# Kernel optimization log

Hardware: AMD Instinct MI355X
Metric: run time of the kernel (lower is better)

## Reference

```python
import jax, jax.numpy as jnp
import numpy as np

NHEAD = 16

def setup_inputs() -> dict:
    key = jax.random.key(0)
    k0, k1, k2, k3 = jax.random.split(key, 4)
    d = 2048
    hd = d // NHEAD
    x = jax.random.normal(k0, (4, 2048, d), dtype=jnp.float32)
    Wq = jax.random.normal(k1, (d, d), dtype=jnp.float32) * (d ** -0.5)
    Wkv = jax.random.normal(k2, (d, 2 * hd), dtype=jnp.float32) * (d ** -0.5)
    Wo = jax.random.normal(k3, (d, d), dtype=jnp.float32) * (d ** -0.5)
    return {"x": x, "Wq": Wq, "Wkv": Wkv, "Wo": Wo}


def reference(x, Wq, Wkv, Wo):
    # Multi-query attention: h query heads share a single K/V head.
    b, n, d = x.shape
    h = NHEAD
    hd = d // h
    scale = hd ** -0.5
    q = (x @ Wq).reshape(b, n, h, hd) * scale      # (b, n, h, hd)
    kv = x @ Wkv                                    # (b, n, 2*hd) -- self-attention (context == input)
    k, v = kv[..., :hd], kv[..., hd:]               # shared single KV head: (b, t, hd)
    sim = jnp.einsum('bnhd,btd->bhnt', q, k)        # (b, h, n, t)
    att = jax.nn.softmax(sim, axis=-1)              # dropout_p = 0.0 (eval)
    y = jnp.einsum('bhnt,btd->bhnd', att, v)        # (b, h, n, hd)
    y = jnp.transpose(y, (0, 2, 1, 3)).reshape(b, n, d)  # 'b h n d -> b n (h d)'
    return y @ Wo
```

## Files before the change

kernel.cpp:

```cpp
#include <hip/hip_runtime.h>

typedef short short8 __attribute__((ext_vector_type(8)));
typedef float f32x4 __attribute__((ext_vector_type(4)));
typedef float f32x16 __attribute__((ext_vector_type(16)));
typedef unsigned int u32x4 __attribute__((ext_vector_type(4)));

#define B_   4
#define N_   2048
#define D_   2048
#define H_   16
#define HD_  128
#define M_   (B_ * N_)
#define KVC  256
#define NQKV (D_ + KVC)

__device__ __forceinline__ unsigned short f2bf(float f) {
  unsigned u = __builtin_bit_cast(unsigned, f);
  u = (u + 0x7FFFu + ((u >> 16) & 1u)) >> 16;
  return (unsigned short)u;
}

__device__ __forceinline__ void gl2lds16(const void* g, void* l) {
  __builtin_amdgcn_global_load_lds((const __attribute__((address_space(1))) void*)g,
                                   (__attribute__((address_space(3))) void*)l,
                                   16, 0, 0);
}

__device__ __forceinline__ unsigned cvt_pk_bf16(float lo, float hi) {
  unsigned r;
  asm volatile("v_cvt_pk_bf16_f32 %0, %1, %2" : "=v"(r) : "v"(lo), "v"(hi));
  return r;
}

#define LGKM0 do { asm volatile("s_waitcnt lgkmcnt(0)" ::: "memory"); \
                   __builtin_amdgcn_sched_barrier(0); } while (0)
#define BAR   do { __builtin_amdgcn_sched_barrier(0); __builtin_amdgcn_s_barrier(); \
                   __builtin_amdgcn_sched_barrier(0); } while (0)

__global__ __launch_bounds__(256) void cvt_bf16_kernel(const float* __restrict__ in,
                                                       unsigned short* __restrict__ out,
                                                       int n8) {
  int i = blockIdx.x * 256 + threadIdx.x;
  if (i >= n8) return;
  float4 a = ((const float4*)in)[i * 2];
  float4 b = ((const float4*)in)[i * 2 + 1];
  u32x4 u;
  u[0] = cvt_pk_bf16(a.x, a.y);
  u[1] = cvt_pk_bf16(a.z, a.w);
  u[2] = cvt_pk_bf16(b.x, b.y);
  u[3] = cvt_pk_bf16(b.z, b.w);
  ((short8*)out)[i] = __builtin_bit_cast(short8, u);
}

__global__ __launch_bounds__(256) void transpose_cvt(const float* __restrict__ in,
                                                     unsigned short* __restrict__ out,
                                                     int R, int C) {
  __shared__ float tile[64][65];
  int r0 = blockIdx.x * 64, c0 = blockIdx.y * 64;
  int t = threadIdx.x;
  int tr = t >> 4, tc4 = (t & 15) * 4;
#pragma unroll
  for (int it = 0; it < 4; ++it) {
    int r = it * 16 + tr;
    float4 v = *(const float4*)(in + (size_t)(r0 + r) * C + c0 + tc4);
    tile[r][tc4 + 0] = v.x; tile[r][tc4 + 1] = v.y;
    tile[r][tc4 + 2] = v.z; tile[r][tc4 + 3] = v.w;
  }
  __syncthreads();
#pragma unroll
  for (int it = 0; it < 4; ++it) {
    int oc = it * 16 + tr;
    ushort4 o;
    o.x = f2bf(tile[tc4 + 0][oc]);
    o.y = f2bf(tile[tc4 + 1][oc]);
    o.z = f2bf(tile[tc4 + 2][oc]);
    o.w = f2bf(tile[tc4 + 3][oc]);
    *(ushort4*)(out + (size_t)(c0 + oc) * R + r0 + tc4) = o;
  }
}

__global__ __launch_bounds__(256) void transpose_v(const unsigned short* __restrict__ kv,
                                                   unsigned short* __restrict__ vt) {
  __shared__ unsigned short tile[64][72];
  int t0 = blockIdx.x * 64, d0 = blockIdx.y * 64, b = blockIdx.z;
  int tid = threadIdx.x;
  int tr = tid >> 3, tc8 = (tid & 7) * 8;
#pragma unroll
  for (int it = 0; it < 2; ++it) {
    int r = it * 32 + tr;
    short8 v = *(const short8*)(kv + (size_t)(b * N_ + t0 + r) * KVC + HD_ + d0 + tc8);
#pragma unroll
    for (int j = 0; j < 8; ++j) tile[r][tc8 + j] = (unsigned short)v[j];
  }
  __syncthreads();
  int beta0 = tc8 >> 2, beta1 = beta0 + 1;
  int p0 = (((beta0 & 3) == 1) || ((beta0 & 3) == 2)) ? (beta0 ^ 3) : beta0;
  int p1 = (((beta1 & 3) == 1) || ((beta1 & 3) == 2)) ? (beta1 ^ 3) : beta1;
#pragma unroll
  for (int it = 0; it < 2; ++it) {
    int od = it * 32 + tr;
    ushort4 lo, hi4;
#pragma unroll
    for (int j = 0; j < 4; ++j) {
      ((unsigned short*)&lo)[j]  = tile[tc8 + j][od];
      ((unsigned short*)&hi4)[j] = tile[tc8 + 4 + j][od];
    }
    unsigned short* base = vt + (size_t)(b * HD_ + d0 + od) * N_ + t0;
    *(ushort4*)(base + p0 * 4) = lo;
    *(ushort4*)(base + p1 * 4) = hi4;
  }
}

template <int MODE>
__global__ __launch_bounds__(512, 2) void gemm256(const unsigned short* __restrict__ A,
                                                  const unsigned short* __restrict__ Bt,
                                                  unsigned short* __restrict__ qb,
                                                  unsigned short* __restrict__ kvb,
                                                  float* __restrict__ fout,
                                                  float sq) {
  constexpr int BK = 64, K = D_, NT = K / BK;
  __shared__ __align__(16) unsigned short lds[2][4][128 * 64];
  const int tid = threadIdx.x;
  const int lane = tid & 63;
  const int w = tid >> 6;
  const int wr = w >> 2, wc = w & 3;
  const int l15 = lane & 15, lg = lane >> 4;
  const int row0 = blockIdx.y * 256, col0 = blockIdx.x * 256;

  f32x4 acc[8][4] = {};
  short8 bf[8];
  short8 af[4];

  auto stage = [&](int buf, int kind, int t) {
    const unsigned short* src = (kind < 2) ? A : Bt;
    const int base = (kind < 2) ? (row0 + kind * 128) : (col0 + (kind - 2) * 128);
#pragma unroll
    for (int ld = 0; ld < 2; ++ld) {
      int e = ld * 512 + tid;
      int r = e >> 3, c = e & 7;
      int csw = c ^ (r & 7);
      gl2lds16(src + (size_t)(base + r) * K + t * BK + csw * 8,
               &lds[buf][kind][(e - lane) * 8]);
    }
  };
  auto readB = [&](int buf) {
#pragma unroll
    for (int n = 0; n < 4; ++n)
#pragma unroll
      for (int kk = 0; kk < 2; ++kk) {
        int row = (wc & 1) * 64 + n * 16 + l15;
        int ch = (kk * 4 + lg) ^ (row & 7);
        bf[n * 2 + kk] = *(const short8*)&lds[buf][2 + (wc >> 1)][row * 64 + ch * 8];
      }
  };
  auto readA = [&](int buf, int q) {
#pragma unroll
    for (int mi = 0; mi < 2; ++mi)
#pragma unroll
      for (int kk = 0; kk < 2; ++kk) {
        int row = (q * 2 + mi) * 16 + l15;
        int ch = (kk * 4 + lg) ^ (row & 7);
        af[mi * 2 + kk] = *(const short8*)&lds[buf][wr][row * 64 + ch * 8];
      }
  };
  auto mfmaQ = [&](int q) {
    __builtin_amdgcn_s_setprio(1);
#pragma unroll
    for (int mi = 0; mi < 2; ++mi)
#pragma unroll
      for (int n = 0; n < 4; ++n)
#pragma unroll
        for (int kk = 0; kk < 2; ++kk)
          acc[q * 2 + mi][n] = __builtin_amdgcn_mfma_f32_16x16x32_bf16(
              af[mi * 2 + kk], bf[n * 2 + kk], acc[q * 2 + mi][n], 0, 0, 0);
    __builtin_amdgcn_s_setprio(0);
  };

  stage(0, 0, 0); stage(0, 1, 0); stage(0, 2, 0); stage(0, 3, 0);
  stage(1, 2, 1); stage(1, 3, 1);

  for (int t = 0; t < NT; t += 2) {
    const bool gY = (t + 2 < NT), gZ = (t + 3 < NT);
    asm volatile("s_waitcnt vmcnt(4)" ::: "memory");
    BAR;
    stage(1, 0, t + 1);
    readB(0); readA(0, 0);
    LGKM0; mfmaQ(0); BAR;
    stage(1, 1, t + 1);
    readA(0, 1); LGKM0; mfmaQ(1); BAR;
    if (gY) stage(0, 2, t + 2);
    readA(0, 2); LGKM0; mfmaQ(2); BAR;
    if (gY) stage(0, 3, t + 2);
    readA(0, 3); LGKM0; mfmaQ(3); BAR;
    if (gZ) { asm volatile("s_waitcnt vmcnt(4)" ::: "memory"); }
    else    { asm volatile("s_waitcnt vmcnt(0)" ::: "memory"); }
    BAR;
    if (gY) stage(0, 0, t + 2);
    readB(1); readA(1, 0);
    LGKM0; mfmaQ(0); BAR;
    if (gY) stage(0, 1, t + 2);
    readA(1, 1); LGKM0; mfmaQ(1); BAR;
    if (gZ) stage(1, 2, t + 3);
    readA(1, 2); LGKM0; mfmaQ(2); BAR;
    if (gZ) stage(1, 3, t + 3);
    readA(1, 3); LGKM0; mfmaQ(3); BAR;
  }

  if (MODE == 0) {
    const bool isq = (col0 < D_);
    unsigned short* outp = isq ? qb : kvb;
    const int ncols = isq ? D_ : KVC;
    const int cbase = isq ? col0 : 0;
    const float sc = isq ? sq : 1.0f;
#pragma unroll
    for (int m = 0; m < 8; ++m)
#pragma unroll
      for (int n = 0; n < 4; ++n)
#pragma unroll
        for (int r = 0; r < 4; ++r) {
          int row = row0 + wr * 128 + m * 16 + lg * 4 + r;
          int col = cbase + wc * 64 + n * 16 + l15;
          outp[(size_t)row * ncols + col] = f2bf(acc[m][n][r] * sc);
        }
  } else {
#pragma unroll
    for (int m = 0; m < 8; ++m)
#pragma unroll
      for (int n = 0; n < 4; ++n)
#pragma unroll
        for (int r = 0; r < 4; ++r) {
          int row = row0 + wr * 128 + m * 16 + lg * 4 + r;
          int col = col0 + wc * 64 + n * 16 + l15;
          fout[(size_t)row * D_ + col] = acc[m][n][r];
        }
  }
}

__global__ __launch_bounds__(256, 2) void attn_kernel(const unsigned short* __restrict__ Q,
                                                      const unsigned short* __restrict__ KV,
                                                      const unsigned short* __restrict__ VT,
                                                      unsigned short* __restrict__ Y) {
  __shared__ __align__(16) unsigned short Ks[64 * HD_];
  __shared__ __align__(16) unsigned short Vs[HD_ * 64];
  const int tid = threadIdx.x;
  const int lane = tid & 63, w = tid >> 6;
  const int l31 = lane & 31, hi = lane >> 5;
  const int ksw = l31 & 7;
  const int qt = blockIdx.x, h = blockIdx.y, b = blockIdx.z;
  const int q0 = qt * 128 + w * 32;

  short8 qf[8];
  {
    const unsigned short* qp = Q + (size_t)(b * N_ + q0 + l31) * D_ + h * HD_ + hi * 8;
#pragma unroll
    for (int kk = 0; kk < 8; ++kk) qf[kk] = *(const short8*)(qp + kk * 16);
  }

  f32x16 o[4] = {};
  float l_r = 0.f;

  for (int t0 = 0; t0 < N_; t0 += 64) {
    __syncthreads();
#pragma unroll
    for (int s = 0; s < 4; ++s) {
      int e = s * 256 + tid;
      int r = e >> 4, c = e & 15;
      int csw = c ^ (r & 7);
      gl2lds16(KV + (size_t)(b * N_ + t0 + r) * KVC + csw * 8, Ks + (e - lane) * 8);
    }
#pragma unroll
    for (int s = 0; s < 4; ++s) {
      int e = s * 256 + tid;
      int r = e >> 3, c = e & 7;
      int csw = c ^ (r & 7);
      gl2lds16(VT + (size_t)(b * HD_ + r) * N_ + t0 + csw * 8, Vs + (e - lane) * 8);
    }
    __syncthreads();

    f32x16 s0 = {}, s1 = {};
    __builtin_amdgcn_s_setprio(1);
#pragma unroll
    for (int kk = 0; kk < 8; ++kk) {
      int ch = ((2 * kk + hi) ^ ksw) * 8;
      short8 kf0 = *(const short8*)&Ks[(l31) * HD_ + ch];
      short8 kf1 = *(const short8*)&Ks[(32 + l31) * HD_ + ch];
      s0 = __builtin_amdgcn_mfma_f32_32x32x16_bf16(kf0, qf[kk], s0, 0, 0, 0);
      s1 = __builtin_amdgcn_mfma_f32_32x32x16_bf16(kf1, qf[kk], s1, 0, 0, 0);
    }
    __builtin_amdgcn_s_setprio(0);

#pragma unroll
    for (int r = 0; r < 16; ++r) {
      s0[r] = __builtin_amdgcn_exp2f(s0[r]);
      s1[r] = __builtin_amdgcn_exp2f(s1[r]);
    }
    float tsum[16];
#pragma unroll
    for (int r = 0; r < 16; ++r) tsum[r] = s0[r] + s1[r];
#pragma unroll
    for (int st = 8; st > 0; st >>= 1)
#pragma unroll
      for (int i = 0; i < 8; ++i) if (i < st) tsum[i] += tsum[i + st];
    l_r += tsum[0] + __shfl_xor(tsum[0], 32);

    unsigned pw0[8], pw1[8];
#pragma unroll
    for (int j = 0; j < 8; ++j) {
      pw0[j] = cvt_pk_bf16(s0[2 * j], s0[2 * j + 1]);
      pw1[j] = cvt_pk_bf16(s1[2 * j], s1[2 * j + 1]);
    }
    short8 paf[4];
    { u32x4 u; u[0]=pw0[0]; u[1]=pw0[1]; u[2]=pw0[2]; u[3]=pw0[3]; paf[0]=__builtin_bit_cast(short8,u); }
    { u32x4 u; u[0]=pw0[4]; u[1]=pw0[5]; u[2]=pw0[6]; u[3]=pw0[7]; paf[1]=__builtin_bit_cast(short8,u); }
    { u32x4 u; u[0]=pw1[0]; u[1]=pw1[1]; u[2]=pw1[2]; u[3]=pw1[3]; paf[2]=__builtin_bit_cast(short8,u); }
    { u32x4 u; u[0]=pw1[4]; u[1]=pw1[5]; u[2]=pw1[6]; u[3]=pw1[7]; paf[3]=__builtin_bit_cast(short8,u); }

    __builtin_amdgcn_s_setprio(1);
#pragma unroll
    for (int ts2 = 0; ts2 < 4; ++ts2) {
#pragma unroll
      for (int dn = 0; dn < 4; ++dn) {
        int row = dn * 32 + l31;
        int ch = ((2 * ts2 + hi) ^ (row & 7)) * 8;
        short8 vf = *(const short8*)&Vs[row * 64 + ch];
        o[dn] = __builtin_amdgcn_mfma_f32_32x32x16_bf16(paf[ts2], vf, o[dn], 0, 0, 0);
      }
    }
    __builtin_amdgcn_s_setprio(0);
  }

  float linv = 1.0f / l_r;
#pragma unroll
  for (int r = 0; r < 16; ++r) {
    int qrow = (r & 3) + 8 * (r >> 2) + 4 * hi;
    float li = __shfl(linv, qrow);
    size_t rowg = (size_t)(b * N_ + q0 + qrow) * D_ + h * HD_;
#pragma unroll
    for (int dn = 0; dn < 4; ++dn)
      Y[rowg + dn * 32 + l31] = f2bf(o[dn][r] * li);
  }
}

extern "C" void kernel_launch(void* const* d_in, const int* in_sizes, int n_in,
                              void* d_out, int out_size, void* d_ws, size_t ws_size,
                              hipStream_t stream) {
  const float* x   = (const float*)d_in[0];
  const float* Wq  = (const float*)d_in[1];
  const float* Wkv = (const float*)d_in[2];
  const float* Wo  = (const float*)d_in[3];

  unsigned char* ws = (unsigned char*)d_ws;
  size_t off = 0;
  auto alloc = [&](size_t bytes) { void* p = ws + off; off += bytes; return p; };
  unsigned short* xb   = (unsigned short*)alloc((size_t)M_ * D_ * 2);
  unsigned short* wqt  = (unsigned short*)alloc((size_t)D_ * D_ * 2);
  unsigned short* wkvt = (unsigned short*)alloc((size_t)KVC * D_ * 2);
  unsigned short* wot  = (unsigned short*)alloc((size_t)D_ * D_ * 2);
  unsigned short* qb   = (unsigned short*)alloc((size_t)M_ * D_ * 2);
  unsigned short* kvb  = (unsigned short*)alloc((size_t)M_ * KVC * 2);
  unsigned short* vt   = (unsigned short*)alloc((size_t)B_ * HD_ * N_ * 2);
  (void)ws_size; (void)in_sizes; (void)n_in; (void)out_size;

  cvt_bf16_kernel<<<(M_ * D_ / 8 + 255) / 256, 256, 0, stream>>>(x, xb, M_ * D_ / 8);
  transpose_cvt<<<dim3(D_ / 64, D_ / 64), 256, 0, stream>>>(Wq, wqt, D_, D_);
  transpose_cvt<<<dim3(D_ / 64, KVC / 64), 256, 0, stream>>>(Wkv, wkvt, D_, KVC);
  transpose_cvt<<<dim3(D_ / 64, D_ / 64), 256, 0, stream>>>(Wo, wot, D_, D_);

  const float scale = 0.12751743f;
  gemm256<0><<<dim3(NQKV / 256, M_ / 256), 512, 0, stream>>>(xb, wqt, qb, kvb, nullptr, scale);
  transpose_v<<<dim3(N_ / 64, HD_ / 64, B_), 256, 0, stream>>>(kvb, vt);

  unsigned short* yb = xb;
  attn_kernel<<<dim3(N_ / 128, H_, B_), 256, 0, stream>>>(qb, kvb, vt, yb);

  gemm256<1><<<dim3(D_ / 256, M_ / 256), 512, 0, stream>>>(yb, wot, nullptr, nullptr,
                                                           (float*)d_out, 1.0f);
}
```

Measured before the change: 328.0 us.

## Load attention K/V fragments directly from global memory and merge weight transposes

The attention kernel stops staging K and V tiles through shared memory with barriers and reads MFMA fragments straight from global memory (via L2/L1), relying on the shared single KV head being reused heavily across query heads. The launch-bounds occupancy hint is also dropped. Separately, the three weight transpose-convert launches become one kernel that picks its matrix from blockIdx.y, saving launch overhead. The trade is fewer barriers and less LDS traffic against per-wave uncoalesced 16-byte global loads with higher latency and cache pressure.

```diff
diff --git a/kernel.cpp b/kernel.cpp
--- a/kernel.cpp
+++ b/kernel.cpp
@@ -52,11 +52,19 @@
   ((short8*)out)[i] = __builtin_bit_cast(short8, u);
 }
 
-__global__ __launch_bounds__(256) void transpose_cvt(const float* __restrict__ in,
-                                                     unsigned short* __restrict__ out,
-                                                     int R, int C) {
+__global__ __launch_bounds__(256) void transpose_cvt3(const float* __restrict__ Wq,
+                                                      const float* __restrict__ Wkv,
+                                                      const float* __restrict__ Wo,
+                                                      unsigned short* __restrict__ wqt,
+                                                      unsigned short* __restrict__ wkvt,
+                                                      unsigned short* __restrict__ wot) {
   __shared__ float tile[64][65];
-  int r0 = blockIdx.x * 64, c0 = blockIdx.y * 64;
+  const float* in; unsigned short* out; int C, cy;
+  if (blockIdx.y < 32)      { in = Wq;  out = wqt;  C = D_;  cy = blockIdx.y; }
+  else if (blockIdx.y < 36) { in = Wkv; out = wkvt; C = KVC; cy = blockIdx.y - 32; }
+  else                      { in = Wo;  out = wot;  C = D_;  cy = blockIdx.y - 36; }
+  const int R = D_;
+  int r0 = blockIdx.x * 64, c0 = cy * 64;
   int t = threadIdx.x;
   int tr = t >> 4, tc4 = (t & 15) * 4;
 #pragma unroll
@@ -236,16 +244,13 @@
   }
 }
 
-__global__ __launch_bounds__(256, 2) void attn_kernel(const unsigned short* __restrict__ Q,
-                                                      const unsigned short* __restrict__ KV,
-                                                      const unsigned short* __restrict__ VT,
-                                                      unsigned short* __restrict__ Y) {
-  __shared__ __align__(16) unsigned short Ks[64 * HD_];
-  __shared__ __align__(16) unsigned short Vs[HD_ * 64];
+__global__ __launch_bounds__(256) void attn_kernel(const unsigned short* __restrict__ Q,
+                                                   const unsigned short* __restrict__ KV,
+                                                   const unsigned short* __restrict__ VT,
+                                                   unsigned short* __restrict__ Y) {
   const int tid = threadIdx.x;
   const int lane = tid & 63, w = tid >> 6;
   const int l31 = lane & 31, hi = lane >> 5;
-  const int ksw = l31 & 7;
   const int qt = blockIdx.x, h = blockIdx.y, b = blockIdx.z;
   const int q0 = qt * 128 + w * 32;
 
@@ -256,34 +261,22 @@
     for (int kk = 0; kk < 8; ++kk) qf[kk] = *(const short8*)(qp + kk * 16);
   }
 
+  const unsigned short* kb0 = KV + (size_t)(b * N_ + l31) * KVC + hi * 8;
+  const unsigned short* kb1 = KV + (size_t)(b * N_ + 32 + l31) * KVC + hi * 8;
+  const unsigned short* vb = VT + (size_t)(b * HD_ + l31) * N_ + hi * 8;
+
   f32x16 o[4] = {};
   float l_r = 0.f;
 
   for (int t0 = 0; t0 < N_; t0 += 64) {
-    __syncthreads();
-#pragma unroll
-    for (int s = 0; s < 4; ++s) {
-      int e = s * 256 + tid;
-      int r = e >> 4, c = e & 15;
-      int csw = c ^ (r & 7);
-      gl2lds16(KV + (size_t)(b * N_ + t0 + r) * KVC + csw * 8, Ks + (e - lane) * 8);
-    }
-#pragma unroll
-    for (int s = 0; s < 4; ++s) {
-      int e = s * 256 + tid;
-      int r = e >> 3, c = e & 7;
-      int csw = c ^ (r & 7);
-      gl2lds16(VT + (size_t)(b * HD_ + r) * N_ + t0 + csw * 8, Vs + (e - lane) * 8);
-    }
-    __syncthreads();
-
     f32x16 s0 = {}, s1 = {};
+    const unsigned short* k0 = kb0 + (size_t)t0 * KVC;
+    const unsigned short* k1 = kb1 + (size_t)t0 * KVC;
     __builtin_amdgcn_s_setprio(1);
 #pragma unroll
     for (int kk = 0; kk < 8; ++kk) {
-      int ch = ((2 * kk + hi) ^ ksw) * 8;
-      short8 kf0 = *(const short8*)&Ks[(l31) * HD_ + ch];
-      short8 kf1 = *(const short8*)&Ks[(32 + l31) * HD_ + ch];
+      short8 kf0 = *(const short8*)(k0 + kk * 16);
+      short8 kf1 = *(const short8*)(k1 + kk * 16);
       s0 = __builtin_amdgcn_mfma_f32_32x32x16_bf16(kf0, qf[kk], s0, 0, 0, 0);
       s1 = __builtin_amdgcn_mfma_f32_32x32x16_bf16(kf1, qf[kk], s1, 0, 0, 0);
     }
@@ -320,9 +313,7 @@
     for (int ts2 = 0; ts2 < 4; ++ts2) {
 #pragma unroll
       for (int dn = 0; dn < 4; ++dn) {
-        int row = dn * 32 + l31;
-        int ch = ((2 * ts2 + hi) ^ (row & 7)) * 8;
-        short8 vf = *(const short8*)&Vs[row * 64 + ch];
+        short8 vf = *(const short8*)(vb + (size_t)(dn * 32) * N_ + t0 + ts2 * 16);
         o[dn] = __builtin_amdgcn_mfma_f32_32x32x16_bf16(paf[ts2], vf, o[dn], 0, 0, 0);
       }
     }
@@ -362,9 +353,7 @@
   (void)ws_size; (void)in_sizes; (void)n_in; (void)out_size;
 
   cvt_bf16_kernel<<<(M_ * D_ / 8 + 255) / 256, 256, 0, stream>>>(x, xb, M_ * D_ / 8);
-  transpose_cvt<<<dim3(D_ / 64, D_ / 64), 256, 0, stream>>>(Wq, wqt, D_, D_);
-  transpose_cvt<<<dim3(D_ / 64, KVC / 64), 256, 0, stream>>>(Wkv, wkvt, D_, KVC);
-  transpose_cvt<<<dim3(D_ / 64, D_ / 64), 256, 0, stream>>>(Wo, wot, D_, D_);
+  transpose_cvt3<<<dim3(32, 68), 256, 0, stream>>>(Wq, Wkv, Wo, wqt, wkvt, wot);
 
   const float scale = 0.12751743f;
   gemm256<0><<<dim3(NQKV / 256, M_ / 256), 512, 0, stream>>>(xb, wqt, qb, kvb, nullptr, scale);
```

Result: slower. 639.3 us (+94.9%).
